# Performance work log

Measured on AMD Instinct MI355X. Metric: run time of the kernel, lower is better.

Reference implementation:

```python
import jax, jax.numpy as jnp
import numpy as np

DIM = 128
IND_DIM = 5
HEADS = 4
DIM_HEAD = 32
HIDDEN = HEADS * DIM_HEAD  # 128
SCALE = DIM_HEAD ** -0.5


def setup_inputs() -> dict:
    key = jax.random.key(0)
    ks = jax.random.split(key, 6)
    b, n = 1, 512
    x = jax.random.normal(ks[0], (b, DIM, n), dtype=jnp.float32)
    indicator = jax.random.normal(ks[1], (b, IND_DIM, n, n), dtype=jnp.float32)
    # conv1d kernels with kernel_size=1 are just (out, in) matrices
    w_qkv = jax.random.normal(ks[2], (HIDDEN * 3, DIM), dtype=jnp.float32) * (DIM ** -0.5)
    w_ind = jax.random.normal(ks[3], (HIDDEN * 2, IND_DIM), dtype=jnp.float32) * (IND_DIM ** -0.5)
    w_out = jax.random.normal(ks[4], (DIM, HIDDEN), dtype=jnp.float32) * (HIDDEN ** -0.5)
    b_out = jax.random.normal(ks[5], (DIM,), dtype=jnp.float32) * 0.01
    return {"x": x, "indicator": indicator, "w_qkv": w_qkv,
            "w_ind": w_ind, "w_out": w_out, "b_out": b_out}


def reference(x, indicator, w_qkv, w_ind, w_out, b_out):
    b, c, n = x.shape
    h, dh = HEADS, DIM_HEAD
    # pointwise conv = channel matmul
    qkv = jnp.einsum('oc,bcn->bon', w_qkv, x)  # (b, 3*hidden, n)
    q, k, v = jnp.split(qkv, 3, axis=1)
    q = q.reshape(b, h, dh, n)
    k = k.reshape(b, h, dh, n)
    v = v.reshape(b, h, dh, n)
    ind = jnp.einsum('oc,bcij->boij', w_ind, indicator)  # (b, 2*hidden, n, n)
    ind_q, ind_k = jnp.split(ind, 2, axis=1)
    ind_q = ind_q.reshape(b, h, dh, n, n)
    ind_k = ind_k.reshape(b, h, dh, n, n)
    qq = (q[..., :, None] + ind_q) * SCALE        # (b, h, dh, n, n)
    kk = k[..., None, :] + ind_k                   # (b, h, dh, n, n)
    sim = jnp.einsum('bhdij,bhdij->bhij', qq, kk)  # (b, h, n, n)
    attn = jax.nn.softmax(sim, axis=-1)
    out = jnp.einsum('bhij,bhdj->bhdi', attn, v)   # (b, h, dh, n)
    out = out.reshape(b, h * dh, n)
    return jnp.einsum('oc,bcn->bon', w_out, out) + b_out[None, :, None]
```

## Files before the change

kernel.cpp:

```cpp
#include <hip/hip_runtime.h>
#include <hip/hip_fp16.h>
#include <math.h>

#define N      512
#define DIMC   128
#define HEADS  4
#define DH     32
#define INDC   5
#define SCALE  0.1767766952966369f

#define QKV_ROWS 384
#define AQ_BASE  384
#define AK_BASE  404
#define TOT_ROWS 424
#define NROW_BLK (TOT_ROWS / 4)

#define MHS_F    (TOT_ROWS * N / 2)
#define WOUTT_F  (MHS_F + 128)

__global__ __launch_bounds__(256) void pre_kernel(const float* __restrict__ w_qkv,
                                                  const float* __restrict__ w_ind,
                                                  const float* __restrict__ x,
                                                  const float* __restrict__ w_out,
                                                  const float* __restrict__ b_out,
                                                  float* __restrict__ out,
                                                  float* __restrict__ ws) {
    const int bx = blockIdx.x;
    const int t  = threadIdx.x;
    __half* rows  = (__half*)ws;
    float* MhS    = ws + MHS_F;
    float* w_outT = ws + WOUTT_F;

    if (bx == NROW_BLK + 1) {
        const int i = blockIdx.y * 256 + t;
        for (int o = 0; o < DIMC; ++o) out[o * N + i] = b_out[o];
        return;
    }
    if (bx == NROW_BLK) {
        if (blockIdx.y != 0) return;
        if (t < HEADS * INDC * INDC) {
            const int h = t / 25, idx = t % 25, c = idx / 5, cc = idx % 5;
            float acc = 0.f;
            for (int d = 0; d < DH; ++d)
                acc = fmaf(w_ind[(h * DH + d) * INDC + c],
                           w_ind[(DIMC + h * DH + d) * INDC + cc], acc);
            MhS[h * 32 + idx] = acc;
        }
        for (int idx = t; idx < DIMC * DIMC; idx += 256) {
            const int o = idx >> 7, c = idx & 127;
            w_outT[c * DIMC + o] = w_out[idx];
        }
        return;
    }

    __shared__ float ws2[4 * DIMC];
    const int o0 = bx * 4;
    for (int idx = t; idx < 4 * DIMC; idx += 256) {
        const int r = idx & 3, m = idx >> 2;
        const int row = o0 + r;
        float val;
        if (row < QKV_ROWS) {
            val = w_qkv[row * DIMC + m];
        } else if (row < AK_BASE) {
            const int rr = row - AQ_BASE, h = rr / INDC, c = rr % INDC;
            float acc = 0.f;
            for (int d = 0; d < DH; ++d)
                acc = fmaf(w_qkv[(h * DH + d) * DIMC + m],
                           w_ind[(DIMC + h * DH + d) * INDC + c], acc);
            val = acc;
        } else {
            const int rr = row - AK_BASE, h = rr / INDC, c = rr % INDC;
            float acc = 0.f;
            for (int d = 0; d < DH; ++d)
                acc = fmaf(w_qkv[(DIMC + h * DH + d) * DIMC + m],
                           w_ind[(h * DH + d) * INDC + c], acc);
            val = acc;
        }
        ws2[m * 4 + r] = val;
    }
    __syncthreads();

    const int i = blockIdx.y * 256 + t;
    float acc[4] = {0.f, 0.f, 0.f, 0.f};
#pragma unroll 8
    for (int c = 0; c < DIMC; ++c) {
        const float xv = x[c * N + i];
        const float4 wv = *(const float4*)(ws2 + c * 4);
        acc[0] = fmaf(wv.x, xv, acc[0]);
        acc[1] = fmaf(wv.y, xv, acc[1]);
        acc[2] = fmaf(wv.z, xv, acc[2]);
        acc[3] = fmaf(wv.w, xv, acc[3]);
    }
#pragma unroll
    for (int r = 0; r < 4; ++r) rows[(o0 + r) * N + i] = __float2half(acc[r]);
}

__global__ __launch_bounds__(256) void attn_kernel(const float* __restrict__ ws,
                                                   const float* __restrict__ ind,
                                                   float* __restrict__ out) {
    const int i0   = blockIdx.x * 2;
    const int h    = blockIdx.y;
    const int t    = threadIdx.x;
    const int lane = t & 63;
    const int wave = t >> 6;

    const __half* rows  = (const __half*)ws;
    const float* MhS    = ws + MHS_F;
    const float* w_outT = ws + WOUTT_F;

    const __half* q  = rows;
    const __half* Aq = rows + 3 * DIMC * N;

    __shared__ float qs[2][DH];
    __shared__ float aqs[2][INDC];
    __shared__ float ms[INDC * INDC];
    __shared__ float ps[2][N];
    __shared__ float red4[2][2][4];
    __shared__ float attv[2][DH];

    if (t < DH)            qs[0][t]      = __half2float(q[(h * DH + t) * N + i0]);
    else if (t < 2 * DH)   qs[1][t - DH] = __half2float(q[(h * DH + t - DH) * N + i0 + 1]);
    else if (t < 2 * DH + INDC)
        aqs[0][t - 2 * DH] = __half2float(Aq[(h * INDC + t - 2 * DH) * N + i0]);
    else if (t < 2 * DH + 2 * INDC)
        aqs[1][t - 2 * DH - INDC] = __half2float(Aq[(h * INDC + t - 2 * DH - INDC) * N + i0 + 1]);
    else if (t >= 96 && t < 96 + 25)
        ms[t - 96] = MhS[h * 32 + (t - 96)];
    __syncthreads();

    float2 ic0[INDC], ic1[INDC];
#pragma unroll
    for (int c = 0; c < INDC; ++c) {
        ic0[c] = ((const float2*)(ind + (c * N + i0) * N))[t];
        ic1[c] = ((const float2*)(ind + (c * N + i0 + 1) * N))[t];
    }

    const __half2* k2  = (const __half2*)(rows + DIMC * N);
    const __half2* Ak2 = (const __half2*)(rows + (3 * DIMC + HEADS * INDC) * N);

    float2 qk0 = {0.f, 0.f}, qk1 = {0.f, 0.f};
#pragma unroll
    for (int d = 0; d < DH; ++d) {
        const float2 kv = __half22float2(k2[(h * DH + d) * 256 + t]);
        const float q0 = qs[0][d], q1 = qs[1][d];
        qk0.x = fmaf(q0, kv.x, qk0.x); qk0.y = fmaf(q0, kv.y, qk0.y);
        qk1.x = fmaf(q1, kv.x, qk1.x); qk1.y = fmaf(q1, kv.y, qk1.y);
    }
    float2 lin0 = {0.f, 0.f}, lin1 = {0.f, 0.f};
#pragma unroll
    for (int c = 0; c < INDC; ++c) {
        const float2 akv = __half22float2(Ak2[(h * INDC + c) * 256 + t]);
        const float a0 = aqs[0][c], a1 = aqs[1][c];
        lin0.x = fmaf(a0 + akv.x, ic0[c].x, lin0.x);
        lin0.y = fmaf(a0 + akv.y, ic0[c].y, lin0.y);
        lin1.x = fmaf(a1 + akv.x, ic1[c].x, lin1.x);
        lin1.y = fmaf(a1 + akv.y, ic1[c].y, lin1.y);
    }
    float2 qd0 = {0.f, 0.f}, qd1 = {0.f, 0.f};
#pragma unroll
    for (int c = 0; c < INDC; ++c) {
        float2 t0 = {0.f, 0.f}, t1 = {0.f, 0.f};
#pragma unroll
        for (int cc = 0; cc < INDC; ++cc) {
            const float mv = ms[c * INDC + cc];
            t0.x = fmaf(mv, ic0[cc].x, t0.x); t0.y = fmaf(mv, ic0[cc].y, t0.y);
            t1.x = fmaf(mv, ic1[cc].x, t1.x); t1.y = fmaf(mv, ic1[cc].y, t1.y);
        }
        qd0.x = fmaf(ic0[c].x, t0.x, qd0.x); qd0.y = fmaf(ic0[c].y, t0.y, qd0.y);
        qd1.x = fmaf(ic1[c].x, t1.x, qd1.x); qd1.y = fmaf(ic1[c].y, t1.y, qd1.y);
    }
    const float s0x = SCALE * (qk0.x + lin0.x + qd0.x);
    const float s0y = SCALE * (qk0.y + lin0.y + qd0.y);
    const float s1x = SCALE * (qk1.x + lin1.x + qd1.x);
    const float s1y = SCALE * (qk1.y + lin1.y + qd1.y);

    float m0 = fmaxf(s0x, s0y), m1 = fmaxf(s1x, s1y);
#pragma unroll
    for (int off = 32; off; off >>= 1) {
        m0 = fmaxf(m0, __shfl_down(m0, off, 64));
        m1 = fmaxf(m1, __shfl_down(m1, off, 64));
    }
    if (lane == 0) { red4[0][0][wave] = m0; red4[0][1][wave] = m1; }
    __syncthreads();
    m0 = fmaxf(fmaxf(red4[0][0][0], red4[0][0][1]), fmaxf(red4[0][0][2], red4[0][0][3]));
    m1 = fmaxf(fmaxf(red4[0][1][0], red4[0][1][1]), fmaxf(red4[0][1][2], red4[0][1][3]));
    const float e0x = __expf(s0x - m0), e0y = __expf(s0y - m0);
    const float e1x = __expf(s1x - m1), e1y = __expf(s1y - m1);
    float su0 = e0x + e0y, su1 = e1x + e1y;
#pragma unroll
    for (int off = 32; off; off >>= 1) {
        su0 += __shfl_down(su0, off, 64);
        su1 += __shfl_down(su1, off, 64);
    }
    __syncthreads();
    if (lane == 0) { red4[1][0][wave] = su0; red4[1][1][wave] = su1; }
    __syncthreads();
    su0 = (red4[1][0][0] + red4[1][0][1]) + (red4[1][0][2] + red4[1][0][3]);
    su1 = (red4[1][1][0] + red4[1][1][1]) + (red4[1][1][2] + red4[1][1][3]);
    const float r0 = 1.f / su0, r1 = 1.f / su1;
    ((float2*)&ps[0][0])[t] = make_float2(e0x * r0, e0y * r0);
    ((float2*)&ps[1][0])[t] = make_float2(e1x * r1, e1y * r1);
    __syncthreads();

    {
        float acc0[8], acc1[8];
#pragma unroll
        for (int dd = 0; dd < 8; ++dd) { acc0[dd] = 0.f; acc1[dd] = 0.f; }
        const float2* ps0 = (const float2*)&ps[0][0];
        const float2* ps1 = (const float2*)&ps[1][0];
        const __half2* v2 = (const __half2*)(rows + 2 * DIMC * N);
        for (int s = 0; s < 4; ++s) {
            const float2 p0 = ps0[lane + 64 * s];
            const float2 p1 = ps1[lane + 64 * s];
#pragma unroll
            for (int dd = 0; dd < 8; ++dd) {
                const float2 vv =
                    __half22float2(v2[(h * DH + wave * 8 + dd) * 256 + lane + 64 * s]);
                acc0[dd] = fmaf(p0.x, vv.x, fmaf(p0.y, vv.y, acc0[dd]));
                acc1[dd] = fmaf(p1.x, vv.x, fmaf(p1.y, vv.y, acc1[dd]));
            }
        }
#pragma unroll
        for (int dd = 0; dd < 8; ++dd) {
            float a0 = acc0[dd], a1 = acc1[dd];
#pragma unroll
            for (int off = 32; off; off >>= 1) {
                a0 += __shfl_down(a0, off, 64);
                a1 += __shfl_down(a1, off, 64);
            }
            if (lane == 0) { attv[0][wave * 8 + dd] = a0; attv[1][wave * 8 + dd] = a1; }
        }
    }
    __syncthreads();

    {
        const int o = t & 127, ii = t >> 7;
        float acc = 0.f;
#pragma unroll 8
        for (int cc = 0; cc < DH; ++cc)
            acc = fmaf(w_outT[(h * DH + cc) * DIMC + o], attv[ii][cc], acc);
        atomicAdd(&out[o * N + i0 + ii], acc);
    }
}

extern "C" void kernel_launch(void* const* d_in, const int* in_sizes, int n_in,
                              void* d_out, int out_size, void* d_ws, size_t ws_size,
                              hipStream_t stream) {
    const float* x         = (const float*)d_in[0];
    const float* indicator = (const float*)d_in[1];
    const float* w_qkv     = (const float*)d_in[2];
    const float* w_ind     = (const float*)d_in[3];
    const float* w_out     = (const float*)d_in[4];
    const float* b_out     = (const float*)d_in[5];
    float* out = (float*)d_out;
    float* ws  = (float*)d_ws;

    pre_kernel<<<dim3(NROW_BLK + 2, 2), 256, 0, stream>>>(w_qkv, w_ind, x, w_out,
                                                          b_out, out, ws);
    attn_kernel<<<dim3(N / 2, HEADS), 256, 0, stream>>>(ws, indicator, out);
}
```

Measured before the change: 107.3 us.

## Move output projection into a separate kernel instead of atomic accumulation

The attention kernel now writes per-head attention outputs to a workspace buffer rather than atomically adding projected results into the output. A new outproj_kernel then does the full 128x128 projection per position and adds the bias, which removes the bias-initialisation blocks from pre_kernel. This is meant to eliminate atomic contention and the separate bias-fill pass. The cost is an extra kernel launch and a round trip of intermediates through memory.

```diff
diff --git a/kernel.cpp b/kernel.cpp
--- a/kernel.cpp
+++ b/kernel.cpp
@@ -17,13 +17,12 @@
 
 #define MHS_F    (TOT_ROWS * N / 2)
 #define WOUTT_F  (MHS_F + 128)
+#define ATT_F    (WOUTT_F + DIMC * DIMC)
 
 __global__ __launch_bounds__(256) void pre_kernel(const float* __restrict__ w_qkv,
                                                   const float* __restrict__ w_ind,
                                                   const float* __restrict__ x,
                                                   const float* __restrict__ w_out,
-                                                  const float* __restrict__ b_out,
-                                                  float* __restrict__ out,
                                                   float* __restrict__ ws) {
     const int bx = blockIdx.x;
     const int t  = threadIdx.x;
@@ -31,11 +30,6 @@
     float* MhS    = ws + MHS_F;
     float* w_outT = ws + WOUTT_F;
 
-    if (bx == NROW_BLK + 1) {
-        const int i = blockIdx.y * 256 + t;
-        for (int o = 0; o < DIMC; ++o) out[o * N + i] = b_out[o];
-        return;
-    }
     if (bx == NROW_BLK) {
         if (blockIdx.y != 0) return;
         if (t < HEADS * INDC * INDC) {
@@ -95,18 +89,18 @@
     for (int r = 0; r < 4; ++r) rows[(o0 + r) * N + i] = __float2half(acc[r]);
 }
 
-__global__ __launch_bounds__(256) void attn_kernel(const float* __restrict__ ws,
+__global__ __launch_bounds__(256) void attn_kernel(const float* __restrict__ ws_c,
                                                    const float* __restrict__ ind,
-                                                   float* __restrict__ out) {
+                                                   float* __restrict__ ws_w) {
     const int i0   = blockIdx.x * 2;
     const int h    = blockIdx.y;
     const int t    = threadIdx.x;
     const int lane = t & 63;
     const int wave = t >> 6;
 
-    const __half* rows  = (const __half*)ws;
-    const float* MhS    = ws + MHS_F;
-    const float* w_outT = ws + WOUTT_F;
+    const __half* rows  = (const __half*)ws_c;
+    const float* MhS    = ws_c + MHS_F;
+    float* att          = ws_w + ATT_F;
 
     const __half* q  = rows;
     const __half* Aq = rows + 3 * DIMC * N;
@@ -233,14 +227,27 @@
     }
     __syncthreads();
 
-    {
-        const int o = t & 127, ii = t >> 7;
-        float acc = 0.f;
+    if (t < 2 * DH) {
+        const int ii = t >> 5, d = t & 31;
+        att[(i0 + ii) * DIMC + h * DH + d] = attv[ii][d];
+    }
+}
+
+__global__ __launch_bounds__(128) void outproj_kernel(const float* __restrict__ ws,
+                                                      const float* __restrict__ b_out,
+                                                      float* __restrict__ out) {
+    const int i = blockIdx.x;
+    const int t = threadIdx.x;
+    const float* w_outT = ws + WOUTT_F;
+    const float* att    = ws + ATT_F;
+    __shared__ float av[DIMC];
+    av[t] = att[i * DIMC + t];
+    __syncthreads();
+    float acc = 0.f;
 #pragma unroll 8
-        for (int cc = 0; cc < DH; ++cc)
-            acc = fmaf(w_outT[(h * DH + cc) * DIMC + o], attv[ii][cc], acc);
-        atomicAdd(&out[o * N + i0 + ii], acc);
-    }
+    for (int c = 0; c < DIMC; ++c)
+        acc = fmaf(w_outT[c * DIMC + t], av[c], acc);
+    out[t * N + i] = acc + b_out[t];
 }
 
 extern "C" void kernel_launch(void* const* d_in, const int* in_sizes, int n_in,
@@ -255,7 +262,7 @@
     float* out = (float*)d_out;
     float* ws  = (float*)d_ws;
 
-    pre_kernel<<<dim3(NROW_BLK + 2, 2), 256, 0, stream>>>(w_qkv, w_ind, x, w_out,
-                                                          b_out, out, ws);
-    attn_kernel<<<dim3(N / 2, HEADS), 256, 0, stream>>>(ws, indicator, out);
-}
+    pre_kernel<<<dim3(NROW_BLK + 1, 2), 256, 0, stream>>>(w_qkv, w_ind, x, w_out, ws);
+    attn_kernel<<<dim3(N / 2, HEADS), 256, 0, stream>>>(ws, indicator, ws);
+    outproj_kernel<<<N, 128, 0, stream>>>(ws, b_out, out);
+}
```

New measurement: 103.4 us. 1.04x faster.
